# Performance work log

Hardware: AMD Instinct MI355X
Metric: run time of the kernel (lower is better)

The kernel has to match this reference:

```python
import jax, jax.numpy as jnp
import numpy as np

ALPHA = -10.0  # softmax sharpness on |x - bin| distances
TAU = 0.0
TAU2 = 0.0
EPS = 1e-10

B, F, L, K = 32, 64, 1024, 32


def setup_inputs() -> dict:
    key = jax.random.key(0)
    k1, k2 = jax.random.split(key)
    x = jax.random.normal(k1, (B, F, L), dtype=jnp.float32)
    bins = jax.random.normal(k2, (K,), dtype=jnp.float32)
    return {"x": x, "bins": bins}


def reference(x, bins):
    # dist: [B, F, L, K] = |x[..., None] - bins|
    dist = jnp.abs(x[..., None] - bins)
    # soft assignment over the K bins (training path of the module)
    soft = jax.nn.softmax(ALPHA * dist, axis=-1)
    assignment = soft + EPS

    # weighted quantization loss: sum of per-bin mean of sqrt(assignment)
    quant = jnp.sum(jnp.mean(jnp.sqrt(assignment), axis=(0, 1, 2)))
    weighted_quant_loss = jnp.stack([quant, jnp.float32(TAU2)])[None, :]  # [1, 2]

    # code entropy of average assignment distribution
    p = jnp.mean(assignment, axis=(0, 1, 2))  # [K]
    code_entropy = -jnp.sum(p * jnp.log(p))
    weighted_code_entropy = jnp.stack([code_entropy, jnp.float32(TAU)])[None, :]  # [1, 2]

    # soft reconstruction against the bins: [B, F, L]
    bit_code = jnp.einsum('bflk,k->bfl', assignment, bins)
    return bit_code, weighted_code_entropy, weighted_quant_loss
```

## Files before the change

### kernel.cpp

```cpp
#include <hip/hip_runtime.h>

#define K      32
#define KH     16
#define TPB    256
#define NB     2048
#define EPT    8
#define NTOT   (32 * 64 * 1024)
#define PSTRIDE (NB * (TPB / 2))

__device__ __forceinline__ float wave_reduce_sum(float v) {
#pragma unroll
  for (int m = 1; m < 64; m <<= 1) v += __shfl_xor(v, m, 64);
  return v;
}

__device__ __forceinline__ float dpp_xor1_add(float v) {
  int sw = __builtin_amdgcn_update_dpp(0, __builtin_bit_cast(int, v),
                                       0xB1, 0xF, 0xF, true);
  return v + __builtin_bit_cast(float, sw);
}
__device__ __forceinline__ float dpp_xor2_add(float v) {
  int sw = __builtin_amdgcn_update_dpp(0, __builtin_bit_cast(int, v),
                                       0x4E, 0xF, 0xF, true);
  return v + __builtin_bit_cast(float, sw);
}
__device__ __forceinline__ float dpp_xor8_add(float v) {
  int sw = __builtin_amdgcn_update_dpp(0, __builtin_bit_cast(int, v),
                                       0x128, 0xF, 0xF, true);
  return v + __builtin_bit_cast(float, sw);
}

__device__ __forceinline__ float pair_lane_reduce(float v) {
  v = dpp_xor2_add(v);
  v += __shfl_xor(v, 4, 64);
  v = dpp_xor8_add(v);
  v += __shfl_xor(v, 16, 64);
  v += __shfl_xor(v, 32, 64);
  return v;
}

__global__ __launch_bounds__(TPB)
void ssq_main(const float* __restrict__ x, const float* __restrict__ bins,
              float* __restrict__ out, float* __restrict__ partials) {
  const int tid  = threadIdx.x;
  const int half = tid & 1;
  const int pslot = blockIdx.x * (TPB / 2) + (tid >> 1);

  float binv[KH];
#pragma unroll
  for (int j = 0; j < KH; ++j) binv[j] = bins[KH * half + j];
  float bs_local = 0.f;
#pragma unroll
  for (int j = 0; j < KH; ++j) bs_local += binv[j];
  const float binsum = dpp_xor1_add(bs_local);
  const float epsb = 1e-10f * binsum;

  float sAcc[KH];
#pragma unroll
  for (int j = 0; j < KH; ++j) sAcc[j] = 0.f;
  float q = 0.f;

  const float Ch = -7.213475204444817f;

  float xv_cur = x[pslot];

#pragma unroll 1
  for (int e = 0; e < EPT; ++e) {
    const float xv = xv_cur;
    if (e + 1 < EPT) xv_cur = x[pslot + (e + 1) * PSTRIDE];
    float t[KH];
    float s0 = 0.f, s1 = 0.f, s2 = 0.f, s3 = 0.f;
    float h0 = 0.f, h1 = 0.f, h2 = 0.f, h3 = 0.f;
    float b0 = 0.f, b1 = 0.f, b2 = 0.f, b3 = 0.f;
#pragma unroll
    for (int j = 0; j < KH; j += 4) {
      float ha = __builtin_amdgcn_exp2f(Ch * fabsf(xv - binv[j + 0]));
      float hb = __builtin_amdgcn_exp2f(Ch * fabsf(xv - binv[j + 1]));
      float hc = __builtin_amdgcn_exp2f(Ch * fabsf(xv - binv[j + 2]));
      float hd = __builtin_amdgcn_exp2f(Ch * fabsf(xv - binv[j + 3]));
      float ta = ha * ha, tb = hb * hb, tc = hc * hc, td = hd * hd;
      t[j + 0] = ta; t[j + 1] = tb; t[j + 2] = tc; t[j + 3] = td;
      s0 += ta; s1 += tb; s2 += tc; s3 += td;
      h0 += ha; h1 += hb; h2 += hc; h3 += hd;
      b0 = fmaf(ta, binv[j + 0], b0);
      b1 = fmaf(tb, binv[j + 1], b1);
      b2 = fmaf(tc, binv[j + 2], b2);
      b3 = fmaf(td, binv[j + 3], b3);
    }
    const float s_loc = (s0 + s1) + (s2 + s3);
    const float b_loc = (b0 + b1) + (b2 + b3);
    const float s_full = dpp_xor1_add(s_loc);
    const float b_full = dpp_xor1_add(b_loc);
    const float inv = __builtin_amdgcn_rcpf(s_full);
    q = fmaf((h0 + h1) + (h2 + h3), __builtin_amdgcn_rsqf(s_full), q);
    if (half == 0) out[pslot + e * PSTRIDE] = fmaf(b_full, inv, epsb);
#pragma unroll
    for (int j = 0; j < KH; ++j) sAcc[j] = fmaf(t[j], inv, sAcc[j]);
  }

  __shared__ float red[4][K + 1];
  const int lane = tid & 63, wv = tid >> 6;
#pragma unroll
  for (int j = 0; j < KH; ++j) {
    float v = pair_lane_reduce(sAcc[j]);
    if (lane < 2) red[wv][KH * lane + j] = v;
  }
  {
    float v = wave_reduce_sum(q);
    if (lane == 0) red[wv][K] = v;
  }
  __syncthreads();
  if (tid < K + 1) {
    float v = red[0][tid] + red[1][tid] + red[2][tid] + red[3][tid];
    partials[tid * NB + blockIdx.x] = v;
  }
}

__global__ __launch_bounds__(TPB)
void ssq_reduce(const float* __restrict__ partials, float* __restrict__ sums) {
  const float* p = partials + blockIdx.x * NB;
  const int tid  = threadIdx.x;
  float s = 0.f;
#pragma unroll
  for (int j = 0; j < NB / TPB; ++j) s += p[tid + j * TPB];
  s = wave_reduce_sum(s);
  __shared__ float red[4];
  if ((tid & 63) == 0) red[tid >> 6] = s;
  __syncthreads();
  if (tid == 0) sums[blockIdx.x] = red[0] + red[1] + red[2] + red[3];
}

__global__ void ssq_final(const float* __restrict__ sums, float* __restrict__ out) {
  const int lane = threadIdx.x;
  float e = 0.f;
  if (lane < K) {
    float p = sums[lane] * (1.0f / (float)NTOT) + 1e-10f;
    e = -p * __logf(p);
  }
  e = wave_reduce_sum(e);
  if (lane == 0) {
    out[NTOT + 0] = e;
    out[NTOT + 1] = 0.f;
    out[NTOT + 2] = sums[K] * (1.0f / (float)NTOT);
    out[NTOT + 3] = 0.f;
  }
}

extern "C" void kernel_launch(void* const* d_in, const int* in_sizes, int n_in,
                              void* d_out, int out_size, void* d_ws, size_t ws_size,
                              hipStream_t stream) {
  const float* x    = (const float*)d_in[0];
  const float* bins = (const float*)d_in[1];
  float* out        = (float*)d_out;
  float* partials   = (float*)d_ws;
  float* sums       = partials + (K + 1) * NB;

  ssq_main  <<<NB,    TPB, 0, stream>>>(x, bins, out, partials);
  ssq_reduce<<<K + 1, TPB, 0, stream>>>(partials, sums);
  ssq_final <<<1,     64,  0, stream>>>(sums, out);
}
```

Measured before the change: 82.30 us.

## Split each element's bins across four lanes instead of two

Each element's 32 bins are now spread over four lanes of 8 bins each, up from two lanes of 16. Elements per thread double to keep the same grid, and launch bounds request 8 blocks per CU. The point is to cut register use per thread, raising occupancy and the overlap of global-memory latency. In exchange each element costs an extra DPP cross-lane add, and per-lane exp work is spread thinner, so 4 lanes now redundantly issue the same x load, the rcp and the rsq.

```diff
diff --git a/kernel.cpp b/kernel.cpp
--- a/kernel.cpp
+++ b/kernel.cpp
@@ -1,12 +1,12 @@
 #include <hip/hip_runtime.h>
 
 #define K      32
-#define KH     16
+#define KQ     8
 #define TPB    256
 #define NB     2048
-#define EPT    8
+#define EPT    16
 #define NTOT   (32 * 64 * 1024)
-#define PSTRIDE (NB * (TPB / 2))
+#define PSTRIDE (NB * (TPB / 4))
 
 __device__ __forceinline__ float wave_reduce_sum(float v) {
 #pragma unroll
@@ -30,8 +30,7 @@
   return v + __builtin_bit_cast(float, sw);
 }
 
-__device__ __forceinline__ float pair_lane_reduce(float v) {
-  v = dpp_xor2_add(v);
+__device__ __forceinline__ float quad_lane_reduce(float v) {
   v += __shfl_xor(v, 4, 64);
   v = dpp_xor8_add(v);
   v += __shfl_xor(v, 16, 64);
@@ -39,71 +38,65 @@
   return v;
 }
 
-__global__ __launch_bounds__(TPB)
+__global__ __launch_bounds__(TPB, 8)
 void ssq_main(const float* __restrict__ x, const float* __restrict__ bins,
               float* __restrict__ out, float* __restrict__ partials) {
-  const int tid  = threadIdx.x;
-  const int half = tid & 1;
-  const int pslot = blockIdx.x * (TPB / 2) + (tid >> 1);
+  const int tid   = threadIdx.x;
+  const int quarter = tid & 3;
+  const int qslot = blockIdx.x * (TPB / 4) + (tid >> 2);
 
-  float binv[KH];
+  float binv[KQ];
 #pragma unroll
-  for (int j = 0; j < KH; ++j) binv[j] = bins[KH * half + j];
+  for (int j = 0; j < KQ; ++j) binv[j] = bins[KQ * quarter + j];
   float bs_local = 0.f;
 #pragma unroll
-  for (int j = 0; j < KH; ++j) bs_local += binv[j];
-  const float binsum = dpp_xor1_add(bs_local);
+  for (int j = 0; j < KQ; ++j) bs_local += binv[j];
+  const float binsum = dpp_xor2_add(dpp_xor1_add(bs_local));
   const float epsb = 1e-10f * binsum;
 
-  float sAcc[KH];
+  float sAcc[KQ];
 #pragma unroll
-  for (int j = 0; j < KH; ++j) sAcc[j] = 0.f;
+  for (int j = 0; j < KQ; ++j) sAcc[j] = 0.f;
   float q = 0.f;
 
   const float Ch = -7.213475204444817f;
 
-  float xv_cur = x[pslot];
+  float xv_cur = x[qslot];
 
 #pragma unroll 1
   for (int e = 0; e < EPT; ++e) {
     const float xv = xv_cur;
-    if (e + 1 < EPT) xv_cur = x[pslot + (e + 1) * PSTRIDE];
-    float t[KH];
-    float s0 = 0.f, s1 = 0.f, s2 = 0.f, s3 = 0.f;
-    float h0 = 0.f, h1 = 0.f, h2 = 0.f, h3 = 0.f;
-    float b0 = 0.f, b1 = 0.f, b2 = 0.f, b3 = 0.f;
+    if (e + 1 < EPT) xv_cur = x[qslot + (e + 1) * PSTRIDE];
+    float t[KQ];
+    float s0 = 0.f, s1 = 0.f, h0 = 0.f, h1 = 0.f, b0 = 0.f, b1 = 0.f;
 #pragma unroll
-    for (int j = 0; j < KH; j += 4) {
+    for (int j = 0; j < KQ; j += 2) {
       float ha = __builtin_amdgcn_exp2f(Ch * fabsf(xv - binv[j + 0]));
       float hb = __builtin_amdgcn_exp2f(Ch * fabsf(xv - binv[j + 1]));
-      float hc = __builtin_amdgcn_exp2f(Ch * fabsf(xv - binv[j + 2]));
-      float hd = __builtin_amdgcn_exp2f(Ch * fabsf(xv - binv[j + 3]));
-      float ta = ha * ha, tb = hb * hb, tc = hc * hc, td = hd * hd;
-      t[j + 0] = ta; t[j + 1] = tb; t[j + 2] = tc; t[j + 3] = td;
-      s0 += ta; s1 += tb; s2 += tc; s3 += td;
-      h0 += ha; h1 += hb; h2 += hc; h3 += hd;
+      float ta = ha * ha, tb = hb * hb;
+      t[j + 0] = ta; t[j + 1] = tb;
+      s0 += ta; s1 += tb;
+      h0 += ha; h1 += hb;
       b0 = fmaf(ta, binv[j + 0], b0);
       b1 = fmaf(tb, binv[j + 1], b1);
-      b2 = fmaf(tc, binv[j + 2], b2);
-      b3 = fmaf(td, binv[j + 3], b3);
     }
-    const float s_loc = (s0 + s1) + (s2 + s3);
-    const float b_loc = (b0 + b1) + (b2 + b3);
-    const float s_full = dpp_xor1_add(s_loc);
-    const float b_full = dpp_xor1_add(b_loc);
+    const float s_loc = s0 + s1;
+    const float b_loc = b0 + b1;
+    const float s_full = dpp_xor2_add(dpp_xor1_add(s_loc));
+    const float b_full = dpp_xor2_add(dpp_xor1_add(b_loc));
     const float inv = __builtin_amdgcn_rcpf(s_full);
-    q = fmaf((h0 + h1) + (h2 + h3), __builtin_amdgcn_rsqf(s_full), q);
-    if (half == 0) out[pslot + e * PSTRIDE] = fmaf(b_full, inv, epsb);
+    q = fmaf(h0 + h1, __builtin_amdgcn_rsqf(s_full), q);
+    if (quarter == 0) out[qslot + e * PSTRIDE] = fmaf(b_full, inv, epsb);
 #pragma unroll
-    for (int j = 0; j < KH; ++j) sAcc[j] = fmaf(t[j], inv, sAcc[j]);
+    for (int j = 0; j < KQ; ++j) sAcc[j] = fmaf(t[j], inv, sAcc[j]);
   }
 
   __shared__ float red[4][K + 1];
   const int lane = tid & 63, wv = tid >> 6;
 #pragma unroll
-  for (int j = 0; j < KH; ++j) {
-    float v = pair_lane_reduce(sAcc[j]);
-    if (lane < 2) red[wv][KH * lane + j] = v;
+  for (int j = 0; j < KQ; ++j) {
+    float v = quad_lane_reduce(sAcc[j]);
+    if (lane < 4) red[wv][KQ * lane + j] = v;
   }
   {
     float v = wave_reduce_sum(q);
```

After: 82.87 us. No clear change (+0.7%).
